# Kernel optimization log

Measured on AMD Instinct MI355X. Metric: run time of the kernel, lower is better.

The kernel has to match this reference:

```python
import jax, jax.numpy as jnp
import numpy as np

B, D, WIN, SW = 256, 38, 640, 10
S = WIN // SW  # 64 time steps
EPS = 1e-5

def leaky(v):
    return jnp.where(v > 0, v, 0.01 * v)

def _ln(v, g, b):
    mu = v.mean(-1, keepdims=True)
    var = v.var(-1, keepdims=True)
    return g * (v - mu) / jnp.sqrt(var + EPS) + b

def setup_inputs():
    key = jax.random.key(0)
    ks = jax.random.split(key, 24)
    n = lambda k, shp, s=0.05: jax.random.normal(k, shp, jnp.float32) * s
    return {
        'x': jax.random.normal(ks[0], (B, D, WIN), jnp.float32),
        'W1': n(ks[1], (D, 64, SW)), 'b1': n(ks[2], (D, 64)),
        'W2': n(ks[3], (D, 4, 3)), 'b2': n(ks[4], (D, 4)),
        'Wl': n(ks[5], (D, 64, 124)), 'bl': n(ks[6], (D, 64)),
        'Wb1': n(ks[7], (64, 64)), 'bb1': n(ks[8], (64,)),
        'lng': jnp.ones((64,), jnp.float32), 'lnb': jnp.zeros((64,), jnp.float32),
        'Wb2': n(ks[9], (64, 64)), 'bb2': n(ks[10], (64,)),
        'Wq': n(ks[11], (1, 64)), 'bq': n(ks[12], (1,)),
        'Wk': n(ks[13], (D, 64)), 'bk': n(ks[14], (D,)),
        'Wv1': n(ks[15], (D, 32, 64)), 'bv1': n(ks[16], (D, 32)),
        'lnvg': jnp.ones((D, 32), jnp.float32), 'lnvb': jnp.zeros((D, 32), jnp.float32),
        'Wv2': n(ks[17], (D, 32)), 'bv2': n(ks[18], (D,)),
        'Wq2': n(ks[19], (1, 64 * D)), 'bq2': n(ks[20], (1,)),
        'Wk2': n(ks[21], (S, 64 * D)), 'bk2': n(ks[22], (S,)),
    }

def reference(x, W1, b1, W2, b2, Wl, bl, Wb1, bb1, lng, lnb, Wb2, bb2,
              Wq, bq, Wk, bk, Wv1, bv1, lnvg, lnvb, Wv2, bv2, Wq2, bq2, Wk2, bk2):
    Bsz = x.shape[0]
    # FE1: per-channel Conv1d(1,64,k=SW,stride=SW) == window-reshape + per-dim GEMM
    xw = x.reshape(Bsz, D, S, SW)
    f1 = leaky(jnp.einsum('bdsw,dow->bdso', xw, W1) + b1[None, :, None, :])  # [B,D,S,64]
    # FE2: per-channel Conv1d(1,4,k=3,p=1) over the 64 features
    xp = jnp.pad(f1, ((0, 0), (0, 0), (0, 0), (1, 1)))
    win = jnp.stack([xp[..., r:r + 64] for r in range(3)], -1)  # [B,D,S,64,3]
    c = leaky(jnp.einsum('bdstr,dcr->bdsct', win, W2) + b2[None, :, None, :, None])  # [B,D,S,4,64]
    # MaxPool1d(3, stride=2): 64 -> 31
    m = jnp.max(jnp.stack([c[..., s:s + 61:2] for s in range(3)], 0), 0)  # [B,D,S,4,31]
    e = leaky(jnp.einsum('bdsf,dof->bdso', m.reshape(Bsz, D, S, 124), Wl) + bl[None, :, None, :])  # embed [B,D,S,64]
    # BeforeInstanceEncoder (shared), recurrent accumulator == cumsum over time
    h = leaky(_ln(jnp.einsum('bdso,po->bdsp', e, Wb1) + bb1, lng, lnb))
    g = leaky(jnp.einsum('bdsp,qp->bdsq', h, Wb2) + bb2)
    acml = jnp.cumsum(g, axis=2)  # [B,D,S,64]
    wq = jax.nn.sigmoid(jnp.einsum('bdso,o->bds', e, Wq[0]) + bq[0])            # [B,D,S]
    wk = jax.nn.sigmoid(jnp.einsum('bdso,jo->bdsj', acml, Wk) + bk)             # [B,D,S,D]
    att1 = jax.nn.softmax(jnp.einsum('bks,bjsk->bsj', wq, wk) / np.float32(np.sqrt(D)), axis=-1)  # [B,S,D]
    v = leaky(_ln(jnp.einsum('bdso,dho->bdsh', e, Wv1) + bv1[None, :, None, :],
                  lnvg[None, :, None, :], lnvb[None, :, None, :]))
    wv = jax.nn.relu(jnp.einsum('bdsh,dh->bds', v, Wv2) + bv2[None, :, None])   # [B,D,S]
    cont1 = jnp.transpose(wv, (0, 2, 1)) * att1  # [B,S,D]
    contributes1 = cont1[..., None]              # [B,S,D,1]
    output1 = cont1.sum(-1, keepdims=True)       # [B,S,1]
    # bag-level attention over time
    ef = jnp.transpose(e, (0, 2, 1, 3)).reshape(Bsz, S, D * 64)
    wq_a = jax.nn.sigmoid(ef @ Wq2.T + bq2)[..., 0]  # [B,S]
    wk_a = jax.nn.sigmoid(ef @ Wk2.T + bk2)          # [B,S,S]
    att2 = jax.nn.softmax(jnp.einsum('bs,bts->bt', wq_a, wk_a) / np.float32(np.sqrt(WIN)), axis=-1)  # [B,S]
    contributes2 = output1 * att2[..., None]  # [B,S,1]
    output2 = contributes2.sum(1)             # [B,1]
    return (output2, contributes2, contributes1)
```

## Files before the change

kernel.cpp:

```cpp
#include <hip/hip_runtime.h>
#include <math.h>

#define Bv 256
#define Dv 38
#define Sv 64
#define SWv 10
#define EPSv 1e-5f

typedef float f4 __attribute__((ext_vector_type(4)));

__device__ __forceinline__ float leaky(float v){ return v > 0.f ? v : 0.01f*v; }
__device__ __forceinline__ float sigm(float v){ return 1.f/(1.f+expf(-v)); }

__device__ __forceinline__ float wred64(float v){
  #pragma unroll
  for (int off=32; off; off>>=1) v += __shfl_xor(v, off, 64);
  return v;
}
__device__ __forceinline__ float wmax64(float v){
  #pragma unroll
  for (int off=32; off; off>>=1) v = fmaxf(v, __shfl_xor(v, off, 64));
  return v;
}

__global__ __launch_bounds__(256) void k0_pack(
    const float* __restrict__ Wl, const float* __restrict__ W1,
    const float* __restrict__ Wv1,
    float* __restrict__ wlT, float* __restrict__ w1T, float* __restrict__ wv1T)
{
  int idx = blockIdx.x*256 + threadIdx.x;
  if (idx < 330752) {
    int d = idx / 8704, r = idx % 8704;
    int c = r / 1088, rr = r % 1088;
    int q = rr / 68, o = rr % 68;
    int ch = q >> 2, io = q & 3, fi = 4*c + io;
    float v = 0.f;
    if (o < 64 && fi <= 30) v = Wl[d*7936 + o*124 + ch*31 + fi];
    wlT[idx] = v;
  } else if (idx < 330752 + 25840) {
    int t = idx - 330752;
    int d = t / 680, rr = t % 680;
    int w = rr / 68, o = rr % 68;
    w1T[t] = (o < 64) ? W1[d*640 + o*10 + w] : 0.f;
  } else if (idx < 330752 + 25840 + 87552) {
    int t = idx - 330752 - 25840;
    int d = t / 2304, rr = t % 2304;
    int o = rr / 36, h = rr % 36;
    wv1T[t] = (h < 32) ? Wv1[d*2048 + h*64 + o] : 0.f;
  }
}

__global__ __launch_bounds__(256, 3) void k1_fe4(
    const float* __restrict__ x,
    const float* __restrict__ w1T_all, const float* __restrict__ b1,
    const float* __restrict__ W2, const float* __restrict__ b2,
    const float* __restrict__ wlT_all, const float* __restrict__ bl,
    const float* __restrict__ Wq, const float* __restrict__ bq,
    const float* __restrict__ wv1T_all, const float* __restrict__ bv1,
    const float* __restrict__ lnvg, const float* __restrict__ lnvb,
    const float* __restrict__ Wv2, const float* __restrict__ bv2,
    float* __restrict__ e_ws, float* __restrict__ wq2_ws, float* __restrict__ wv_ws)
{
  __shared__ float sm[12368];
  const int d  = blockIdx.x >> 7;
  const int b0 = (blockIdx.x & 127) * 2;
  const int tid = threadIdx.x;
  const int z = tid >> 7;
  const int t = tid & 127;
  const int tx = t & 15, ty = t >> 4;
  const int wz = ty >> 2;
  const int bd = (b0 + z)*Dv + d;
  const float bq0 = bq[0];

#define PJ(j) ((j) < 4 ? 4*ty + (j) : 32 + 4*ty + ((j)-4))

  if (tid < 64) {
    sm[12032+tid] = b1[d*64+tid];
    sm[12096+tid] = bl[d*64+tid];
    sm[12160+tid] = Wq[tid];
  } else if (tid < 96) {
    int u = tid-64;
    sm[12240+u]=bv1[d*32+u]; sm[12272+u]=lnvg[d*32+u];
    sm[12304+u]=lnvb[d*32+u]; sm[12336+u]=Wv2[d*32+u];
  } else if (tid < 108) sm[12224+(tid-96)] = W2[d*12+(tid-96)];
  else if (tid < 112)   sm[12236+(tid-108)] = b2[d*4+(tid-108)];

  {
    const f4* s4 = (const f4*)(w1T_all + (size_t)d*680);
    if (tid < 170) ((f4*)&sm[9792])[tid] = s4[tid];
  }
  for (int i = tid; i < 1280; i += 256) {
    int z2 = i / 640, tt = i % 640;
    sm[10472 + z2*680 + (tt%10)*68 + tt/10] =
      x[((size_t)((b0+z2)*Dv + d))*640 + tt];
  }
  const f4* wlsrc = (const f4*)(wlT_all + (size_t)d*8704);
  {
    ((f4*)&sm[8704])[tid] = wlsrc[tid];
    if (tid < 16) ((f4*)&sm[8704])[tid+256] = wlsrc[tid+256];
  }
  __syncthreads();

  float fe[4][8];
  #pragma unroll
  for (int i=0;i<4;++i)
    #pragma unroll
    for (int j=0;j<8;++j) fe[i][j]=0.f;
  #pragma unroll
  for (int w = 0; w < 10; ++w) {
    f4 a   = *(const f4*)&sm[10472 + z*680 + w*68 + 4*tx];
    f4 blo = *(const f4*)&sm[9792 + w*68 + 4*ty];
    f4 bhi = *(const f4*)&sm[9792 + w*68 + 32 + 4*ty];
    float bv8[8] = {blo[0],blo[1],blo[2],blo[3],bhi[0],bhi[1],bhi[2],bhi[3]};
    #pragma unroll
    for (int i=0;i<4;++i)
      #pragma unroll
      for (int j=0;j<8;++j) fe[i][j] += a[i]*bv8[j];
  }
  #pragma unroll
  for (int j=0;j<8;++j) {
    int o = PJ(j);
    float bb = sm[12032+o];
    f4 v = {leaky(fe[0][j]+bb), leaky(fe[1][j]+bb), leaky(fe[2][j]+bb), leaky(fe[3][j]+bb)};
    *(f4*)&sm[z*4352 + o*68 + 4*tx] = v;
  }
  __syncthreads();

  float ea[4][8];
  #pragma unroll
  for (int i=0;i<4;++i)
    #pragma unroll
    for (int j=0;j<8;++j) ea[i][j]=0.f;

  f4 wr0, wr1;
  for (int c = 0; c < 8; ++c) {
    if (c > 0) {
      ((f4*)&sm[8704])[tid] = wr0;
      if (tid < 16) ((f4*)&sm[8704])[tid+256] = wr1;
    }
    {
      int s = t & 63, ioh = t >> 6;
      float* mdst = &sm[9792 + z*1088];
      const float* fsrc = &sm[z*4352];
      #pragma unroll
      for (int io2=0; io2<2; ++io2) {
        int io = 2*ioh + io2;
        int fi = 4*c + io;
        if (fi <= 30) {
          int t0 = 2*fi - 1;
          float v0 = (t0 < 0) ? 0.f : fsrc[t0*68+s];
          float v1 = fsrc[(t0+1)*68+s];
          float v2 = fsrc[(t0+2)*68+s];
          float v3 = fsrc[(t0+3)*68+s];
          float v4 = fsrc[(t0+4)*68+s];
          #pragma unroll
          for (int ch=0; ch<4; ++ch) {
            float w0=sm[12224+ch*3], w1=sm[12224+ch*3+1], w2=sm[12224+ch*3+2];
            float bb=sm[12236+ch];
            float ca = bb + v0*w0 + v1*w1 + v2*w2;
            float cb = bb + v1*w0 + v2*w1 + v3*w2;
            float cc = bb + v2*w0 + v3*w1 + v4*w2;
            mdst[(ch*4+io)*68+s] = fmaxf(fmaxf(leaky(ca),leaky(cb)),leaky(cc));
          }
        }
      }
    }
    if (c < 7) {
      wr0 = wlsrc[(c+1)*272 + tid];
      if (tid < 16) wr1 = wlsrc[(c+1)*272 + 256 + tid];
    }
    __syncthreads();
    {
      const float* ma = &sm[9792 + z*1088];
      #pragma unroll
      for (int q=0;q<16;++q){
        f4 a   = *(const f4*)&ma[q*68+4*tx];
        f4 blo = *(const f4*)&sm[8704 + q*68+4*ty];
        f4 bhi = *(const f4*)&sm[8704 + q*68+32+4*ty];
        float bv8[8] = {blo[0],blo[1],blo[2],blo[3],bhi[0],bhi[1],bhi[2],bhi[3]};
        #pragma unroll
        for (int i=0;i<4;++i)
          #pragma unroll
          for (int j=0;j<8;++j) ea[i][j] += a[i]*bv8[j];
      }
    }
    __syncthreads();
  }

  float ev[4][8];
  #pragma unroll
  for (int i=0;i<4;++i)
    #pragma unroll
    for (int j=0;j<8;++j) ev[i][j] = leaky(ea[i][j] + sm[12096 + PJ(j)]);

  {
    float* erow = e_ws + (size_t)bd * 4096;
    #pragma unroll
    for (int i=0;i<4;++i) {
      f4 lo = {ev[i][0],ev[i][1],ev[i][2],ev[i][3]};
      f4 hi = {ev[i][4],ev[i][5],ev[i][6],ev[i][7]};
      *(f4*)&erow[(4*tx+i)*64 + 4*ty] = lo;
      *(f4*)&erow[(4*tx+i)*64 + 32 + 4*ty] = hi;
    }
  }
  #pragma unroll
  for (int j=0;j<8;++j) {
    int o = PJ(j);
    f4 v = {ev[0][j],ev[1][j],ev[2][j],ev[3][j]};
    *(f4*)&sm[z*4352 + o*68 + 4*tx] = v;
  }
  #pragma unroll
  for (int i=0;i<4;++i) {
    float p = 0.f;
    #pragma unroll
    for (int j=0;j<8;++j) p += ev[i][j]*sm[12160 + PJ(j)];
    p += __shfl_xor(p, 16);
    p += __shfl_xor(p, 32);
    if ((ty & 3) == 0) sm[11520 + z*128 + wz*64 + 4*tx + i] = p;
  }
  {
    const f4* s4 = (const f4*)(wv1T_all + (size_t)d*2304);
    f4 a0 = s4[tid], a1 = s4[tid+256];
    ((f4*)&sm[8704])[tid] = a0;
    ((f4*)&sm[8704])[tid+256] = a1;
    if (tid < 64) ((f4*)&sm[8704])[tid+512] = s4[tid+512];
  }
  __syncthreads();

  if (tid < 128) {
    int z2 = tid >> 6, r = tid & 63;
    float p = sm[11520 + z2*128 + r] + sm[11520 + z2*128 + 64 + r];
    wq2_ws[((size_t)(b0+z2)*64 + r)*Dv + d] = sigm(p + bq0);
  }

  float va[4][4];
  #pragma unroll
  for (int i=0;i<4;++i)
    #pragma unroll
    for (int j=0;j<4;++j) va[i][j]=0.f;
  #pragma unroll 8
  for (int o = 0; o < 64; ++o) {
    f4 a  = *(const f4*)&sm[z*4352 + o*68 + 4*tx];
    f4 bb = *(const f4*)&sm[8704 + o*36 + 4*ty];
    #pragma unroll
    for (int i=0;i<4;++i)
      #pragma unroll
      for (int j=0;j<4;++j) va[i][j] += a[i]*bb[j];
  }
  #pragma unroll
  for (int i=0;i<4;++i)
    #pragma unroll
    for (int j=0;j<4;++j) va[i][j] += sm[12240 + 4*ty + j];

  #pragma unroll
  for (int i=0;i<4;++i) {
    float ps=0.f, pq=0.f;
    #pragma unroll
    for (int j=0;j<4;++j) { ps += va[i][j]; pq += va[i][j]*va[i][j]; }
    ps += __shfl_xor(ps, 16); ps += __shfl_xor(ps, 32);
    pq += __shfl_xor(pq, 16); pq += __shfl_xor(pq, 32);
    if ((ty & 3) == 0) {
      sm[11008 + z*128 + wz*64 + 4*tx + i] = ps;
      sm[11264 + z*128 + wz*64 + 4*tx + i] = pq;
    }
  }
  __syncthreads();
  if (tid < 128) {
    int z2 = tid >> 6, r = tid & 63;
    float s_ = sm[11008 + z2*128 + r] + sm[11008 + z2*128 + 64 + r];
    float q_ = sm[11264 + z2*128 + r] + sm[11264 + z2*128 + 64 + r];
    float mu = s_*(1.f/32.f);
    float vr = q_*(1.f/32.f) - mu*mu;
    sm[11776 + z2*64 + r] = mu;
    sm[11904 + z2*64 + r] = rsqrtf(vr + EPSv);
  }
  __syncthreads();

  #pragma unroll
  for (int i=0;i<4;++i) {
    float mu = sm[11776 + z*64 + 4*tx + i];
    float rs = sm[11904 + z*64 + 4*tx + i];
    float p = 0.f;
    #pragma unroll
    for (int j=0;j<4;++j) {
      int h = 4*ty + j;
      float vh = leaky(sm[12272+h]*(va[i][j]-mu)*rs + sm[12304+h]);
      p += vh*sm[12336+h];
    }
    p += __shfl_xor(p, 16);
    p += __shfl_xor(p, 32);
    if ((ty & 3) == 0) sm[11520 + z*128 + wz*64 + 4*tx + i] = p;
  }
  __syncthreads();
  if (tid < 128) {
    int z2 = tid >> 6, r = tid & 63;
    float p = sm[11520 + z2*128 + r] + sm[11520 + z2*128 + 64 + r];
    wv_ws[((size_t)((b0+z2)*Dv + d))*64 + r] = fmaxf(p + bv2[d], 0.f);
  }
#undef PJ
}

__global__ __launch_bounds__(256) void k2_fused(
    const float* __restrict__ e_ws,
    const float* __restrict__ Wb1, const float* __restrict__ bb1,
    const float* __restrict__ lng, const float* __restrict__ lnb,
    const float* __restrict__ Wb2, const float* __restrict__ bb2,
    const float* __restrict__ Wk, const float* __restrict__ bk,
    const float* __restrict__ wq2_ws, float* __restrict__ score1)
{
  __shared__ float smem[14080];
  float* bufA = smem;
  float* bufB = smem + 8448;
  float* pts  = smem + 12544;
  float* ptq  = smem + 13184;
  float* stmu = smem + 13824;
  float* strs = smem + 13952;

  const int tid = threadIdx.x;
  const int tx = tid & 31;
  const int ty = tid >> 5;
  const int wid = tid >> 6;
  const int lane = tid & 63;
  const int bd0 = blockIdx.x * 2;
  const int bd1 = bd0 + 1;

#define PJ(j) ((j) < 4 ? 4*ty + (j) : 32 + 4*ty + ((j)-4))

  const int r0 = tid & 15, c0 = tid >> 4;

  f4 w2r[4];
  {
    const f4* W2src = (const f4*)Wb2;
    #pragma unroll
    for (int q = 0; q < 4; ++q) w2r[q] = W2src[(r0+16*q)*16 + c0];
  }

  {
    const f4* Esrc  = (const f4*)(e_ws + (size_t)bd0 * 4096);
    #pragma unroll
    for (int q = 0; q < 8; ++q) {
      int r = r0 + 16*q;
      f4 v = Esrc[r*16 + c0];
      #pragma unroll
      for (int k = 0; k < 4; ++k) bufA[(4*c0+k)*132 + r] = v[k];
    }
    const f4* W1src = (const f4*)Wb1;
    #pragma unroll
    for (int q = 0; q < 4; ++q) {
      int rr = r0 + 16*q;
      f4 v1 = W1src[rr*16 + c0];
      #pragma unroll
      for (int k = 0; k < 4; ++k) bufB[(4*c0+k)*64 + rr] = v1[k];
    }
  }
  __syncthreads();

  float bb1v[8], lngv[8], lnbv[8], bb2v[8];
  #pragma unroll
  for (int j=0;j<8;++j) {
    int p = PJ(j);
    bb1v[j]=bb1[p]; lngv[j]=lng[p]; lnbv[j]=lnb[p]; bb2v[j]=bb2[p];
  }

  float h[4][8];
  #pragma unroll
  for (int i=0;i<4;++i)
    #pragma unroll
    for (int j=0;j<8;++j) h[i][j]=0.f;
  for (int o = 0; o < 64; ++o) {
    f4 a  = *(const f4*)(bufA + o*132 + 4*tx);
    f4 bl = *(const f4*)(bufB + o*64 + 4*ty);
    f4 bh = *(const f4*)(bufB + o*64 + 32 + 4*ty);
    float bv8[8] = {bl[0],bl[1],bl[2],bl[3],bh[0],bh[1],bh[2],bh[3]};
    #pragma unroll
    for (int i=0;i<4;++i)
      #pragma unroll
      for (int j=0;j<8;++j) h[i][j] += a[i]*bv8[j];
  }
  #pragma unroll
  for (int i=0;i<4;++i)
    #pragma unroll
    for (int j=0;j<8;++j) h[i][j] += bb1v[j];

  #pragma unroll
  for (int i=0;i<4;++i) {
    float ps=0.f, pq=0.f;
    #pragma unroll
    for (int j=0;j<8;++j) { ps += h[i][j]; pq += h[i][j]*h[i][j]; }
    ps += __shfl_xor(ps, 32);
    pq += __shfl_xor(pq, 32);
    if (lane < 32) { pts[(4*tx+i)*5 + wid] = ps; ptq[(4*tx+i)*5 + wid] = pq; }
  }
  __syncthreads();

  {
    #pragma unroll
    for (int q = 0; q < 4; ++q) {
      int rr = r0 + 16*q;
      f4 v = w2r[q];
      #pragma unroll
      for (int k = 0; k < 4; ++k) bufB[(4*c0+k)*64 + rr] = v[k];
    }
  }
  float wkr[10];
  #pragma unroll
  for (int n = 0; n < 10; ++n) {
    int i2 = tid + 256*n;
    int q = i2/40, k = i2%40;
    wkr[n] = (k < Dv) ? Wk[k*64 + q] : 0.f;
  }
  if (tid < 128) {
    float s = pts[tid*5]+pts[tid*5+1]+pts[tid*5+2]+pts[tid*5+3];
    float q = ptq[tid*5]+ptq[tid*5+1]+ptq[tid*5+2]+ptq[tid*5+3];
    float mu = s*(1.f/64.f);
    float va = q*(1.f/64.f) - mu*mu;
    stmu[tid] = mu;
    strs[tid] = rsqrtf(va + EPSv);
  }
  __syncthreads();

  {
    float muv[4], rsv[4];
    #pragma unroll
    for (int i=0;i<4;++i) { muv[i]=stmu[4*tx+i]; rsv[i]=strs[4*tx+i]; }
    #pragma unroll
    for (int j=0;j<8;++j) {
      f4 v;
      #pragma unroll
      for (int i=0;i<4;++i)
        v[i] = leaky(lngv[j]*(h[i][j]-muv[i])*rsv[i] + lnbv[j]);
      *(f4*)&bufA[PJ(j)*132 + 4*tx] = v;
    }
  }
  __syncthreads();

  float g[4][8];
  #pragma unroll
  for (int i=0;i<4;++i)
    #pragma unroll
    for (int j=0;j<8;++j) g[i][j]=0.f;
  for (int p = 0; p < 64; ++p) {
    f4 a  = *(const f4*)(bufA + p*132 + 4*tx);
    f4 bl = *(const f4*)(bufB + p*64 + 4*ty);
    f4 bh = *(const f4*)(bufB + p*64 + 32 + 4*ty);
    float bv8[8] = {bl[0],bl[1],bl[2],bl[3],bh[0],bh[1],bh[2],bh[3]};
    #pragma unroll
    for (int i=0;i<4;++i)
      #pragma unroll
      for (int j=0;j<8;++j) g[i][j] += a[i]*bv8[j];
  }
  #pragma unroll
  for (int i=0;i<4;++i)
    #pragma unroll
    for (int j=0;j<8;++j) g[i][j] = leaky(g[i][j] + bb2v[j]);

  #pragma unroll
  for (int j=0;j<8;++j) {
    float c0_=g[0][j], c1=c0_+g[1][j], c2=c1+g[2][j], c3=c2+g[3][j];
    float incl = c3;
    #pragma unroll
    for (int dd=1; dd<16; dd<<=1) {
      float t = __shfl_up(incl, dd, 16);
      if ((tid & 15) >= dd) incl += t;
    }
    float ex = incl - c3;
    g[0][j]=ex+c0_; g[1][j]=ex+c1; g[2][j]=ex+c2; g[3][j]=ex+c3;
  }
  __syncthreads();

  #pragma unroll
  for (int j=0;j<8;++j) {
    f4 v = {g[0][j], g[1][j], g[2][j], g[3][j]};
    *(f4*)&bufA[PJ(j)*132 + 4*tx] = v;
  }
  #pragma unroll
  for (int n = 0; n < 10; ++n) bufB[tid + 256*n] = wkr[n];
  __syncthreads();

  float u[4][4], u2[4][4];
  #pragma unroll
  for (int i=0;i<4;++i)
    #pragma unroll
    for (int j=0;j<4;++j) { u[i][j]=0.f; u2[i][j]=0.f; }
  for (int q = 0; q < 64; ++q) {
    f4 a   = *(const f4*)(bufA + q*132 + 4*tx);
    f4 b1v = *(const f4*)(bufB + q*40 + 4*ty);
    #pragma unroll
    for (int i=0;i<4;++i)
      #pragma unroll
      for (int j=0;j<4;++j) u[i][j] += a[i]*b1v[j];
    if (ty < 2) {
      f4 b2v = *(const f4*)(bufB + q*40 + 32 + 4*ty);
      #pragma unroll
      for (int i=0;i<4;++i)
        #pragma unroll
        for (int j=0;j<4;++j) u2[i][j] += a[i]*b2v[j];
    }
  }

  const int b0g = bd0/Dv, d0g = bd0%Dv, b1g = bd1/Dv, d1g = bd1%Dv;
  #pragma unroll
  for (int i=0;i<4;++i) {
    int r = 4*tx + i;
    int s = r & 63;
    int bb_ = (r >> 6) ? b1g : b0g;
    const float* wqrow = wq2_ws + ((size_t)bb_*Sv + s)*Dv;
    float p = 0.f;
    #pragma unroll
    for (int j=0;j<4;++j) {
      int k = 4*ty + j;
      p += sigm(u[i][j] + bk[k]) * wqrow[k];
    }
    if (ty < 2) {
      #pragma unroll
      for (int j=0;j<4;++j) {
        int k = 32 + 4*ty + j;
        if (k < Dv) p += sigm(u2[i][j] + bk[k]) * wqrow[k];
      }
    }
    p += __shfl_xor(p, 32);
    if (lane < 32) pts[r*5 + wid] = p;
  }
  __syncthreads();
  if (tid < 128) {
    float tot = pts[tid*5]+pts[tid*5+1]+pts[tid*5+2]+pts[tid*5+3];
    int grp = tid >> 6, s = tid & 63;
    int bb_ = grp ? b1g : b0g;
    int dd_ = grp ? d1g : d0g;
    score1[((size_t)bb_*Sv + s)*Dv + dd_] = tot;
  }
#undef PJ
}

__global__ __launch_bounds__(256) void k3_att1(
    const float* __restrict__ score1, const float* __restrict__ wv_ws,
    const float* __restrict__ e_ws, const float* __restrict__ Wq2, const float* __restrict__ bq2,
    float* __restrict__ out_c1, float* __restrict__ output1, float* __restrict__ wq_a)
{
  const int blk = blockIdx.x;
  const int b = blk / Sv, s = blk % Sv;
  const int tid = threadIdx.x;
  const int wid = tid>>6, lane = tid&63;
  __shared__ float red[4];

  if (wid==0) {
    const float invsq = 0.16222142113076254f;
    float sc = (lane<Dv) ? score1[(b*Sv+s)*Dv+lane]*invsq : -1e30f;
    float mx = wmax64(sc);
    float ex = (lane<Dv) ? expf(sc-mx) : 0.f;
    float den = wred64(ex);
    float att = ex/den;
    float c1 = 0.f;
    if (lane<Dv) {
      c1 = wv_ws[(b*Dv+lane)*Sv+s]*att;
      out_c1[(b*Sv+s)*Dv+lane] = c1;
    }
    float tot = wred64(c1);
    if (lane==0) output1[b*Sv+s] = tot;
  }
  float p = 0.f;
  for (int idx=tid; idx<Dv*64; idx+=256) {
    int d = idx>>6, o = idx&63;
    p += e_ws[((size_t)(b*Dv+d)*Sv+s)*64+o]*Wq2[idx];
  }
  p = wred64(p);
  if (lane==0) red[wid]=p;
  __syncthreads();
  if (tid==0) wq_a[b*Sv+s] = sigm(red[0]+red[1]+red[2]+red[3]+bq2[0]);
}

__global__ __launch_bounds__(256) void k4_gemm(
    const float* __restrict__ e_ws, const float* __restrict__ Wk2, const float* __restrict__ bk2,
    const float* __restrict__ wq_a, float* __restrict__ score2)
{
  const int b = blockIdx.x;
  const int tid = threadIdx.x;
  const int tx = tid & 15, ty = tid >> 4;
  __shared__ float AsT[64*68];
  __shared__ float BsT[64*68];
  __shared__ float pt[64*17];

  float acc[4][4];
  #pragma unroll
  for (int i=0;i<4;++i)
    #pragma unroll
    for (int j=0;j<4;++j) acc[i][j]=0.f;

  const int r0 = tid & 15, oc0 = tid >> 4;
  const f4* Bsrc = (const f4*)Wk2;

  for (int d = 0; d < 38; ++d) {
    const f4* Asrc = (const f4*)(e_ws + ((size_t)(b*Dv+d))*4096);
    #pragma unroll
    for (int q = 0; q < 4; ++q) {
      int r = r0 + 16*q;
      f4 av = Asrc[r*16 + oc0];
      f4 bv = Bsrc[(size_t)r*608 + d*16 + oc0];
      #pragma unroll
      for (int k = 0; k < 4; ++k) {
        AsT[(4*oc0+k)*68 + r] = av[k];
        BsT[(4*oc0+k)*68 + r] = bv[k];
      }
    }
    __syncthreads();
    #pragma unroll 4
    for (int o = 0; o < 64; ++o) {
      f4 a  = *(const f4*)&AsT[o*68 + 4*tx];
      f4 bb = *(const f4*)&BsT[o*68 + 4*ty];
      #pragma unroll
      for (int i=0;i<4;++i)
        #pragma unroll
        for (int j=0;j<4;++j) acc[i][j] += a[i]*bb[j];
    }
    __syncthreads();
  }

  #pragma unroll
  for (int i=0;i<4;++i) {
    float p = 0.f;
    #pragma unroll
    for (int j=0;j<4;++j) {
      int s = 4*ty + j;
      p += sigm(acc[i][j] + bk2[s]) * wq_a[b*Sv + s];
    }
    pt[(4*tx+i)*17 + ty] = p;
  }
  __syncthreads();
  if (tid < 64) {
    float tot = 0.f;
    #pragma unroll
    for (int y=0;y<16;++y) tot += pt[tid*17+y];
    score2[b*Sv + tid] = tot;
  }
}

__global__ __launch_bounds__(64) void k5_final(
    const float* __restrict__ score2, const float* __restrict__ output1,
    float* __restrict__ out)
{
  const int b = blockIdx.x;
  const int lane = threadIdx.x;
  const float inv = 0.039528470752104741f;
  float v = score2[b*Sv+lane]*inv;
  float mx = wmax64(v);
  float ex = expf(v-mx);
  float den = wred64(ex);
  float att = ex/den;
  float c2 = output1[b*Sv+lane]*att;
  out[256 + b*Sv + lane] = c2;
  float tot = wred64(c2);
  if (lane==0) out[b] = tot;
}

extern "C" void kernel_launch(void* const* d_in, const int* in_sizes, int n_in,
                              void* d_out, int out_size, void* d_ws, size_t ws_size,
                              hipStream_t stream)
{
  const float* x    = (const float*)d_in[0];
  const float* W1   = (const float*)d_in[1];
  const float* b1   = (const float*)d_in[2];
  const float* W2   = (const float*)d_in[3];
  const float* b2   = (const float*)d_in[4];
  const float* Wl   = (const float*)d_in[5];
  const float* bl   = (const float*)d_in[6];
  const float* Wb1  = (const float*)d_in[7];
  const float* bb1  = (const float*)d_in[8];
  const float* lng  = (const float*)d_in[9];
  const float* lnb  = (const float*)d_in[10];
  const float* Wb2  = (const float*)d_in[11];
  const float* bb2  = (const float*)d_in[12];
  const float* Wq   = (const float*)d_in[13];
  const float* bq   = (const float*)d_in[14];
  const float* Wk   = (const float*)d_in[15];
  const float* bk   = (const float*)d_in[16];
  const float* Wv1  = (const float*)d_in[17];
  const float* bv1  = (const float*)d_in[18];
  const float* lnvg = (const float*)d_in[19];
  const float* lnvb = (const float*)d_in[20];
  const float* Wv2  = (const float*)d_in[21];
  const float* bv2  = (const float*)d_in[22];
  const float* Wq2  = (const float*)d_in[23];
  const float* bq2  = (const float*)d_in[24];
  const float* Wk2  = (const float*)d_in[25];
  const float* bk2  = (const float*)d_in[26];

  float* ws = (float*)d_ws;
  float* e_ws  = ws;
  float* wq2w  = e_ws + (size_t)Bv*Dv*Sv*64;
  float* wv_ws = wq2w + (size_t)Bv*Sv*Dv;
  float* sc1   = wv_ws + (size_t)Bv*Dv*Sv;
  float* out1  = sc1 + (size_t)Bv*Sv*Dv;
  float* wqa   = out1 + (size_t)Bv*Sv;
  float* sc2   = wqa + (size_t)Bv*Sv;
  float* wlT   = sc2 + (size_t)Bv*Sv;
  float* w1T   = wlT + 330752;
  float* wv1T  = w1T + 25840;

  float* out = (float*)d_out;
  float* out_c1 = out + 256 + Bv*Sv;

  hipLaunchKernelGGL(k0_pack, dim3(1736), dim3(256), 0, stream,
    Wl, W1, Wv1, wlT, w1T, wv1T);
  hipLaunchKernelGGL(k1_fe4, dim3(Dv*128), dim3(256), 0, stream,
    x, w1T, b1, W2, b2, wlT, bl, Wq, bq, wv1T, bv1, lnvg, lnvb, Wv2, bv2,
    e_ws, wq2w, wv_ws);
  hipLaunchKernelGGL(k2_fused, dim3(Bv*Dv/2), dim3(256), 0, stream,
    e_ws, Wb1, bb1, lng, lnb, Wb2, bb2, Wk, bk, wq2w, sc1);
  hipLaunchKernelGGL(k3_att1, dim3(Bv*Sv), dim3(256), 0, stream,
    sc1, wv_ws, e_ws, Wq2, bq2, out_c1, out1, wqa);
  hipLaunchKernelGGL(k4_gemm, dim3(Bv), dim3(256), 0, stream,
    e_ws, Wk2, bk2, wqa, sc2);
  hipLaunchKernelGGL(k5_final, dim3(Bv), dim3(64), 0, stream, sc2, out1, out);
}
```

Measured before the change: 703.6 us.

## Fuse Wq2 projection into feature kernel and vectorize conv-maxpool stage

Result: faster. 663.5 us (-5.7%).

```diff
diff --git a/kernel.cpp b/kernel.cpp
--- a/kernel.cpp
+++ b/kernel.cpp
@@ -59,9 +59,11 @@
     const float* __restrict__ wv1T_all, const float* __restrict__ bv1,
     const float* __restrict__ lnvg, const float* __restrict__ lnvb,
     const float* __restrict__ Wv2, const float* __restrict__ bv2,
-    float* __restrict__ e_ws, float* __restrict__ wq2_ws, float* __restrict__ wv_ws)
+    const float* __restrict__ Wq2,
+    float* __restrict__ e_ws, float* __restrict__ wq2_ws, float* __restrict__ wv_ws,
+    float* __restrict__ wqa_p)
 {
-  __shared__ float sm[12368];
+  __shared__ float sm[12688];
   const int d  = blockIdx.x >> 7;
   const int b0 = (blockIdx.x & 127) * 2;
   const int tid = threadIdx.x;
@@ -78,6 +80,7 @@
     sm[12032+tid] = b1[d*64+tid];
     sm[12096+tid] = bl[d*64+tid];
     sm[12160+tid] = Wq[tid];
+    sm[12368+tid] = Wq2[d*64+tid];
   } else if (tid < 96) {
     int u = tid-64;
     sm[12240+u]=bv1[d*32+u]; sm[12272+u]=lnvg[d*32+u];
@@ -111,11 +114,10 @@
     f4 a   = *(const f4*)&sm[10472 + z*680 + w*68 + 4*tx];
     f4 blo = *(const f4*)&sm[9792 + w*68 + 4*ty];
     f4 bhi = *(const f4*)&sm[9792 + w*68 + 32 + 4*ty];
-    float bv8[8] = {blo[0],blo[1],blo[2],blo[3],bhi[0],bhi[1],bhi[2],bhi[3]};
     #pragma unroll
     for (int i=0;i<4;++i)
       #pragma unroll
-      for (int j=0;j<8;++j) fe[i][j] += a[i]*bv8[j];
+      for (int j=0;j<8;++j) fe[i][j] += a[i]*((j<4)?blo[j&3]:bhi[j&3]);
   }
   #pragma unroll
   for (int j=0;j<8;++j) {
@@ -139,29 +141,33 @@
       if (tid < 16) ((f4*)&sm[8704])[tid+256] = wr1;
     }
     {
-      int s = t & 63, ioh = t >> 6;
-      float* mdst = &sm[9792 + z*1088];
-      const float* fsrc = &sm[z*4352];
-      #pragma unroll
-      for (int io2=0; io2<2; ++io2) {
-        int io = 2*ioh + io2;
-        int fi = 4*c + io;
-        if (fi <= 30) {
-          int t0 = 2*fi - 1;
-          float v0 = (t0 < 0) ? 0.f : fsrc[t0*68+s];
-          float v1 = fsrc[(t0+1)*68+s];
-          float v2 = fsrc[(t0+2)*68+s];
-          float v3 = fsrc[(t0+3)*68+s];
-          float v4 = fsrc[(t0+4)*68+s];
+      int sg = t & 15, io = (t >> 4) & 3, chh = t >> 6;
+      int fi = 4*c + io;
+      if (fi <= 30) {
+        int t0 = 2*fi - 1;
+        const float* fsrc = &sm[z*4352];
+        f4 v0;
+        if (fi == 0) { v0[0]=0.f; v0[1]=0.f; v0[2]=0.f; v0[3]=0.f; }
+        else         { v0 = *(const f4*)&fsrc[t0*68 + 4*sg]; }
+        f4 v1 = *(const f4*)&fsrc[(t0+1)*68 + 4*sg];
+        f4 v2 = *(const f4*)&fsrc[(t0+2)*68 + 4*sg];
+        f4 v3 = *(const f4*)&fsrc[(t0+3)*68 + 4*sg];
+        f4 v4 = *(const f4*)&fsrc[(t0+4)*68 + 4*sg];
+        float* mdst = &sm[9792 + z*1088];
+        #pragma unroll
+        for (int cc2 = 0; cc2 < 2; ++cc2) {
+          int ch = 2*chh + cc2;
+          float w0=sm[12224+ch*3], w1=sm[12224+ch*3+1], w2=sm[12224+ch*3+2];
+          float bb=sm[12236+ch];
+          f4 r;
           #pragma unroll
-          for (int ch=0; ch<4; ++ch) {
-            float w0=sm[12224+ch*3], w1=sm[12224+ch*3+1], w2=sm[12224+ch*3+2];
-            float bb=sm[12236+ch];
-            float ca = bb + v0*w0 + v1*w1 + v2*w2;
-            float cb = bb + v1*w0 + v2*w1 + v3*w2;
-            float cc = bb + v2*w0 + v3*w1 + v4*w2;
-            mdst[(ch*4+io)*68+s] = fmaxf(fmaxf(leaky(ca),leaky(cb)),leaky(cc));
+          for (int e2=0;e2<4;++e2) {
+            float ca = bb + v0[e2]*w0 + v1[e2]*w1 + v2[e2]*w2;
+            float cb = bb + v1[e2]*w0 + v2[e2]*w1 + v3[e2]*w2;
+            float cc = bb + v2[e2]*w0 + v3[e2]*w1 + v4[e2]*w2;
+            r[e2] = fmaxf(fmaxf(leaky(ca),leaky(cb)),leaky(cc));
           }
+          *(f4*)&mdst[(ch*4+io)*68 + 4*sg] = r;
         }
       }
     }
@@ -177,11 +183,10 @@
         f4 a   = *(const f4*)&ma[q*68+4*tx];
         f4 blo = *(const f4*)&sm[8704 + q*68+4*ty];
         f4 bhi = *(const f4*)&sm[8704 + q*68+32+4*ty];
-        float bv8[8] = {blo[0],blo[1],blo[2],blo[3],bhi[0],bhi[1],bhi[2],bhi[3]};
         #pragma unroll
         for (int i=0;i<4;++i)
           #pragma unroll
-          for (int j=0;j<8;++j) ea[i][j] += a[i]*bv8[j];
+          for (int j=0;j<8;++j) ea[i][j] += a[i]*((j<4)?blo[j&3]:bhi[j&3]);
       }
     }
     __syncthreads();
@@ -211,12 +216,18 @@
   }
   #pragma unroll
   for (int i=0;i<4;++i) {
-    float p = 0.f;
-    #pragma unroll
-    for (int j=0;j<8;++j) p += ev[i][j]*sm[12160 + PJ(j)];
-    p += __shfl_xor(p, 16);
-    p += __shfl_xor(p, 32);
-    if ((ty & 3) == 0) sm[11520 + z*128 + wz*64 + 4*tx + i] = p;
+    float p = 0.f, pa = 0.f;
+    #pragma unroll
+    for (int j=0;j<8;++j) {
+      p  += ev[i][j]*sm[12160 + PJ(j)];
+      pa += ev[i][j]*sm[12368 + PJ(j)];
+    }
+    p += __shfl_xor(p, 16);  p += __shfl_xor(p, 32);
+    pa += __shfl_xor(pa, 16); pa += __shfl_xor(pa, 32);
+    if ((ty & 3) == 0) {
+      sm[11520 + z*128 + wz*64 + 4*tx + i] = p;
+      sm[12432 + z*128 + wz*64 + 4*tx + i] = pa;
+    }
   }
   {
     const f4* s4 = (const f4*)(wv1T_all + (size_t)d*2304);
@@ -231,6 +242,8 @@
     int z2 = tid >> 6, r = tid & 63;
     float p = sm[11520 + z2*128 + r] + sm[11520 + z2*128 + 64 + r];
     wq2_ws[((size_t)(b0+z2)*64 + r)*Dv + d] = sigm(p + bq0);
+    float pa = sm[12432 + z2*128 + r] + sm[12432 + z2*128 + 64 + r];
+    wqa_p[((size_t)(b0+z2)*64 + r)*Dv + d] = pa;
   }
 
   float va[4][4];
@@ -371,11 +384,10 @@
     f4 a  = *(const f4*)(bufA + o*132 + 4*tx);
     f4 bl = *(const f4*)(bufB + o*64 + 4*ty);
     f4 bh = *(const f4*)(bufB + o*64 + 32 + 4*ty);
-    float bv8[8] = {bl[0],bl[1],bl[2],bl[3],bh[0],bh[1],bh[2],bh[3]};
     #pragma unroll
     for (int i=0;i<4;++i)
       #pragma unroll
-      for (int j=0;j<8;++j) h[i][j] += a[i]*bv8[j];
+      for (int j=0;j<8;++j) h[i][j] += a[i]*((j<4)?bl[j&3]:bh[j&3]);
   }
   #pragma unroll
   for (int i=0;i<4;++i)
@@ -443,11 +455,10 @@
     f4 a  = *(const f4*)(bufA + p*132 + 4*tx);
     f4 bl = *(const f4*)(bufB + p*64 + 4*ty);
     f4 bh = *(const f4*)(bufB + p*64 + 32 + 4*ty);
-    float bv8[8] = {bl[0],bl[1],bl[2],bl[3],bh[0],bh[1],bh[2],bh[3]};
     #pragma unroll
     for (int i=0;i<4;++i)
       #pragma unroll
-      for (int j=0;j<8;++j) g[i][j] += a[i]*bv8[j];
+      for (int j=0;j<8;++j) g[i][j] += a[i]*((j<4)?bl[j&3]:bh[j&3]);
   }
   #pragma unroll
   for (int i=0;i<4;++i)
@@ -532,41 +543,32 @@
 #undef PJ
 }
 
-__global__ __launch_bounds__(256) void k3_att1(
+__global__ __launch_bounds__(64) void k3_att1(
     const float* __restrict__ score1, const float* __restrict__ wv_ws,
-    const float* __restrict__ e_ws, const float* __restrict__ Wq2, const float* __restrict__ bq2,
+    const float* __restrict__ wqa_p, const float* __restrict__ bq2,
     float* __restrict__ out_c1, float* __restrict__ output1, float* __restrict__ wq_a)
 {
   const int blk = blockIdx.x;
   const int b = blk / Sv, s = blk % Sv;
-  const int tid = threadIdx.x;
-  const int wid = tid>>6, lane = tid&63;
-  __shared__ float red[4];
-
-  if (wid==0) {
-    const float invsq = 0.16222142113076254f;
-    float sc = (lane<Dv) ? score1[(b*Sv+s)*Dv+lane]*invsq : -1e30f;
-    float mx = wmax64(sc);
-    float ex = (lane<Dv) ? expf(sc-mx) : 0.f;
-    float den = wred64(ex);
-    float att = ex/den;
-    float c1 = 0.f;
-    if (lane<Dv) {
-      c1 = wv_ws[(b*Dv+lane)*Sv+s]*att;
-      out_c1[(b*Sv+s)*Dv+lane] = c1;
-    }
-    float tot = wred64(c1);
-    if (lane==0) output1[b*Sv+s] = tot;
-  }
-  float p = 0.f;
-  for (int idx=tid; idx<Dv*64; idx+=256) {
-    int d = idx>>6, o = idx&63;
-    p += e_ws[((size_t)(b*Dv+d)*Sv+s)*64+o]*Wq2[idx];
-  }
+  const int lane = threadIdx.x;
+
+  const float invsq = 0.16222142113076254f;
+  float sc = (lane<Dv) ? score1[(b*Sv+s)*Dv+lane]*invsq : -1e30f;
+  float mx = wmax64(sc);
+  float ex = (lane<Dv) ? expf(sc-mx) : 0.f;
+  float den = wred64(ex);
+  float att = ex/den;
+  float c1 = 0.f;
+  if (lane<Dv) {
+    c1 = wv_ws[(b*Dv+lane)*Sv+s]*att;
+    out_c1[(b*Sv+s)*Dv+lane] = c1;
+  }
+  float tot = wred64(c1);
+  if (lane==0) output1[b*Sv+s] = tot;
+
+  float p = (lane < Dv) ? wqa_p[((size_t)b*Sv + s)*Dv + lane] : 0.f;
   p = wred64(p);
-  if (lane==0) red[wid]=p;
-  __syncthreads();
-  if (tid==0) wq_a[b*Sv+s] = sigm(red[0]+red[1]+red[2]+red[3]+bq2[0]);
+  if (lane==0) wq_a[b*Sv+s] = sigm(p + bq2[0]);
 }
 
 __global__ __launch_bounds__(256) void k4_gemm(
@@ -695,6 +697,7 @@
   float* wlT   = sc2 + (size_t)Bv*Sv;
   float* w1T   = wlT + 330752;
   float* wv1T  = w1T + 25840;
+  float* wqap  = wv1T + 87552;
 
   float* out = (float*)d_out;
   float* out_c1 = out + 256 + Bv*Sv;
@@ -703,11 +706,11 @@
     Wl, W1, Wv1, wlT, w1T, wv1T);
   hipLaunchKernelGGL(k1_fe4, dim3(Dv*128), dim3(256), 0, stream,
     x, w1T, b1, W2, b2, wlT, bl, Wq, bq, wv1T, bv1, lnvg, lnvb, Wv2, bv2,
-    e_ws, wq2w, wv_ws);
+    Wq2, e_ws, wq2w, wv_ws, wqap);
   hipLaunchKernelGGL(k2_fused, dim3(Bv*Dv/2), dim3(256), 0, stream,
     e_ws, Wb1, bb1, lng, lnb, Wb2, bb2, Wk, bk, wq2w, sc1);
-  hipLaunchKernelGGL(k3_att1, dim3(Bv*Sv), dim3(256), 0, stream,
-    sc1, wv_ws, e_ws, Wq2, bq2, out_c1, out1, wqa);
+  hipLaunchKernelGGL(k3_att1, dim3(Bv*Sv), dim3(64), 0, stream,
+    sc1, wv_ws, wqap, bq2, out_c1, out1, wqa);
   hipLaunchKernelGGL(k4_gemm, dim3(Bv), dim3(256), 0, stream,
     e_ws, Wk2, bk2, wqa, sc2);
   hipLaunchKernelGGL(k5_final, dim3(Bv), dim3(64), 0, stream, sc2, out1, out);
```
